# Kernel optimization log

Hardware: AMD Instinct MI355X
Metric: run time of the kernel (lower is better)

## Reference

```python
import jax, jax.numpy as jnp
import numpy as np

NSAMPLE = 32
EPS = 1e-5


def _fps(xyz, npoint):
    # xyz: [B, N, 3] -> indices [B, npoint] (farthest point sampling, start at idx 0)
    B, N, _ = xyz.shape
    def body(i, state):
        idx, dist, far = state
        idx = idx.at[:, i].set(far)
        centroid = jnp.take_along_axis(xyz, far[:, None, None], axis=1)  # [B,1,3]
        d = jnp.sum((xyz - centroid) ** 2, axis=-1)                      # [B,N]
        dist = jnp.minimum(dist, d)
        far = jnp.argmax(dist, axis=-1).astype(jnp.int32)
        return idx, dist, far
    idx0 = jnp.zeros((B, npoint), jnp.int32)
    dist0 = jnp.full((B, N), 1e10, xyz.dtype)
    far0 = jnp.zeros((B,), jnp.int32)
    idx, _, _ = jax.lax.fori_loop(0, npoint, body, (idx0, dist0, far0))
    return idx


def _knn(query, ref, k):
    # query [B,S,3], ref [B,N,3] -> neighbor idx [B,S,k]
    d = (jnp.sum(query * query, -1)[:, :, None]
         - 2.0 * jnp.einsum('bsc,bnc->bsn', query, ref)
         + jnp.sum(ref * ref, -1)[:, None, :])
    _, idx = jax.lax.top_k(-d, k)
    return idx


def _gather(x, idx):
    # x [B,N,C], idx [B,S,K] -> [B,S,K,C]
    B, S, K = idx.shape
    out = jnp.take_along_axis(x, idx.reshape(B, S * K)[..., None], axis=1)
    return out.reshape(B, S, K, x.shape[-1])


def _set_abstraction(xyz, feat, npoint, weights):
    # xyz [B,N,3], feat [B,N,C]
    fidx = _fps(xyz, npoint)
    new_xyz = jnp.take_along_axis(xyz, fidx[..., None], axis=1)        # [B,S,3]
    nidx = _knn(new_xyz, xyz, NSAMPLE)                                 # [B,S,K]
    g_xyz = _gather(xyz, nidx) - new_xyz[:, :, None, :]                # [B,S,K,3]
    g_feat = _gather(feat, nidx)                                       # [B,S,K,C]
    x = jnp.concatenate([g_xyz, g_feat], axis=-1)                      # [B,S,K,3+C]
    for W in weights:  # 1x1 conv == per-point matmul, then InstanceNorm2d (affine=False) + ReLU
        x = jnp.einsum('bskc,cd->bskd', x, W)
        mu = jnp.mean(x, axis=(1, 2), keepdims=True)
        var = jnp.var(x, axis=(1, 2), keepdims=True)
        x = jax.nn.relu((x - mu) * jax.lax.rsqrt(var + EPS))
    new_feat = jnp.max(x, axis=2)                                      # [B,S,Cout]
    return new_xyz, new_feat, fidx


def setup_inputs() -> dict:
    key = jax.random.key(0)
    ks = jax.random.split(key, 8)
    B, N = 4, 16384
    pc = jax.random.normal(ks[0], (B, 3, N), jnp.float32)
    feature = jax.random.normal(ks[1], (B, 3, N), jnp.float32)
    def w(k, cin, cout):
        return jax.random.normal(k, (cin, cout), jnp.float32) / np.sqrt(cin).astype(np.float32)
    return {
        'pc': pc, 'feature': feature,
        'sa1_w1': w(ks[2], 6, 32),  'sa1_w2': w(ks[3], 32, 32), 'sa1_w3': w(ks[4], 32, 32),
        'sa2_w1': w(ks[5], 35, 64), 'sa2_w2': w(ks[6], 64, 64), 'sa2_w3': w(ks[7], 64, 64),
    }


def reference(pc, feature, sa1_w1, sa1_w2, sa1_w3, sa2_w1, sa2_w2, sa2_w3):
    NPOINT = 4096
    xyz = jnp.transpose(pc, (0, 2, 1))       # [B,N,3]
    feat = jnp.transpose(feature, (0, 2, 1))  # [B,N,3]
    xyz1, feat1, fidx1 = _set_abstraction(xyz, feat, NPOINT // 2, [sa1_w1, sa1_w2, sa1_w3])
    xyz2, feat2, fidx2 = _set_abstraction(xyz1, feat1, NPOINT // 4, [sa2_w1, sa2_w2, sa2_w3])
    # match torch channel-first layout on outputs
    pc_l1 = jnp.transpose(xyz1, (0, 2, 1))
    pc_l2 = jnp.transpose(xyz2, (0, 2, 1))
    feat_l2 = jnp.transpose(feat2, (0, 2, 1))  # [B,64,NPOINT//4]
    return (pc, pc_l1, pc_l2, feat_l2, fidx1, fidx2)
```

## Files before the change

### kernel.cpp

```cpp
#include <hip/hip_runtime.h>
#include <math.h>

namespace {

constexpr int BB = 4;
constexpr int N0 = 16384;
constexpr int S1 = 2048;
constexpr int S2 = 1024;

__device__ __forceinline__ float sq3(float x, float y, float z){
  #pragma clang fp contract(off)
  return x*x + y*y + z*z;
}
__device__ __forceinline__ float sqdist(float ax,float ay,float az,float bx,float by,float bz){
  #pragma clang fp contract(off)
  float dx = ax-bx; float dy = ay-by; float dz = az-bz;
  return dx*dx + dy*dy + dz*dz;
}
__device__ __forceinline__ float dot3(float ax,float ay,float az,float bx,float by,float bz){
  #pragma clang fp contract(off)
  return ax*bx + ay*by + az*bz;
}
__device__ __forceinline__ float knndist(float qs, float dot, float rs){
  #pragma clang fp contract(off)
  return (qs - 2.0f*dot) + rs;
}

__global__ __launch_bounds__(256) void k_setup(const float* __restrict__ pc,
                                               const float* __restrict__ feat,
                                               float* __restrict__ out_pc,
                                               float* __restrict__ xyz,
                                               float* __restrict__ fN,
                                               float* __restrict__ rsq0)
{
  int t = blockIdx.x*256 + threadIdx.x;
  if (t < BB*3*N0) out_pc[t] = pc[t];
  if (t < BB*N0){
    int b = t >> 14, n = t & (N0-1);
    const float* p = pc + (size_t)b*3*N0;
    float x = p[n], y = p[N0+n], z = p[2*N0+n];
    float* q = xyz + (size_t)t*3;
    q[0]=x; q[1]=y; q[2]=z;
    rsq0[t] = sq3(x,y,z);
    const float* f = feat + (size_t)b*3*N0;
    float* g = fN + (size_t)t*3;
    g[0]=f[n]; g[1]=f[N0+n]; g[2]=f[2*N0+n];
  }
}

__device__ __forceinline__ void fps_writeout(int b, int i, float cx, float cy, float cz, int far,
                                             float* sxyz, float* srsq, float* pcl, float* fidxf, int NP)
{
  fidxf[(size_t)b*NP + i] = (float)far;
  float* o = sxyz + ((size_t)b*NP + i)*3;
  o[0]=cx; o[1]=cy; o[2]=cz;
  float* pb = pcl + (size_t)b*3*NP;
  pb[i] = cx; pb[NP+i] = cy; pb[2*NP+i] = cz;
  srsq[(size_t)b*NP + i] = sq3(cx,cy,cz);
}

template<int N, int NP, int BS, int PPT>
__global__ __launch_bounds__(BS) void k_fps(const float* __restrict__ pts,
                                            float* __restrict__ sxyz,
                                            float* __restrict__ srsq,
                                            float* __restrict__ pcl,
                                            float* __restrict__ fidxf)
{
  static_assert(N == BS*PPT, "bad fps shape");
  int b = blockIdx.x, t = threadIdx.x;
  const float* P = pts + (size_t)b*N*3;
  float px[PPT], py[PPT], pz[PPT], dist[PPT];
  #pragma unroll
  for (int j=0;j<PPT;j++){
    int g = t + BS*j;
    px[j]=P[g*3]; py[j]=P[g*3+1]; pz[j]=P[g*3+2];
    dist[j]=1e10f;
  }
  __shared__ unsigned s_maxbits;
  __shared__ int      s_win;
  __shared__ float    s_lo;
  float cx = P[0], cy = P[1], cz = P[2];
  if (t == 0){
    s_maxbits = 0u;
    s_win = 0x7FFFFFFF;
    fps_writeout(b, 0, cx, cy, cz, 0, sxyz, srsq, pcl, fidxf, NP);
  }
  __syncthreads();
  for (int i=1;i<NP;i++){
    float vmax = -1.0f;
    #pragma unroll
    for (int j=0;j<PPT;j++){
      float d  = sqdist(px[j],py[j],pz[j],cx,cy,cz);
      float nd = fminf(dist[j], d);
      dist[j]  = nd;
      vmax = fmaxf(vmax, nd);
    }
    #pragma unroll
    for (int off=32; off>0; off>>=1) vmax = fmaxf(vmax, __shfl_down(vmax, off));
    if ((t & 63) == 0) atomicMax(&s_maxbits, __float_as_uint(vmax));
    __syncthreads();
    if (t == 0){
      unsigned mb = s_maxbits;
      float s = sqrtf(__uint_as_float(mb));
      unsigned xb = mb;
      while (xb > 0u && sqrtf(__uint_as_float(xb - 1u)) == s) xb--;
      s_lo = __uint_as_float(xb);
      s_maxbits = 0u;
      s_win = 0x7FFFFFFF;
    }
    __syncthreads();
    float lo = s_lo;
    int li = 0x7FFFFFFF;
    #pragma unroll
    for (int j=PPT-1;j>=0;j--) if (dist[j] >= lo) li = t + BS*j;
    if (li != 0x7FFFFFFF) atomicMin(&s_win, li);
    __syncthreads();
    int far = s_win;
    cx = P[(size_t)far*3]; cy = P[(size_t)far*3+1]; cz = P[(size_t)far*3+2];
    if (t == 0) fps_writeout(b, i, cx, cy, cz, far, sxyz, srsq, pcl, fidxf, NP);
  }
}

template<int NREF, int PPT, int NQ>
__global__ __launch_bounds__(512) void k_knn(const float* __restrict__ qxyz,
                                             const float* __restrict__ qrsq,
                                             const float* __restrict__ rxyz,
                                             const float* __restrict__ rrsq,
                                             int* __restrict__ nidx)
{
  static_assert(NREF == 512*PPT, "bad knn shape");
  int q = blockIdx.x;
  int b = q / NQ;
  int t = threadIdx.x;
  const float* R  = rxyz + (size_t)b*NREF*3;
  const float* RS = rrsq + (size_t)b*NREF;
  float qx = qxyz[(size_t)q*3], qy = qxyz[(size_t)q*3+1], qz = qxyz[(size_t)q*3+2];
  float qs = qrsq[q];
  unsigned u[PPT];
  #pragma unroll
  for (int j=0;j<PPT;j++){
    int g = t + 512*j;
    float rx=R[g*3], ry=R[g*3+1], rz=R[g*3+2];
    float d = knndist(qs, dot3(qx,qy,qz,rx,ry,rz), RS[g]);
    unsigned bu = __float_as_uint(d);
    u[j] = ((int)bu < 0) ? ~bu : (bu | 0x80000000u);
  }
  __shared__ unsigned hist[256];
  __shared__ unsigned s_pref, s_pm, s_want, s_cnteq;
  __shared__ int s_n;
  __shared__ int s_eq[1024];
  __shared__ int s_ne;
  if (t == 0){ s_pref=0u; s_pm=0u; s_want=32u; s_n=0; s_ne=0; }

  for (int shift=24; shift>=0; shift-=8){
    if (t < 256) hist[t] = 0u;
    __syncthreads();
    unsigned pref = s_pref, pm = s_pm;
    #pragma unroll
    for (int j=0;j<PPT;j++){
      if ((u[j] & pm) == pref) atomicAdd(&hist[(u[j]>>shift)&255], 1u);
    }
    __syncthreads();
    if (t < 64){
      unsigned h0=hist[4*t], h1=hist[4*t+1], h2=hist[4*t+2], h3=hist[4*t+3];
      unsigned ssum = h0+h1+h2+h3;
      unsigned inc = ssum;
      #pragma unroll
      for (int off=1; off<64; off<<=1){
        unsigned o = __shfl_up(inc, off);
        if (t >= off) inc += o;
      }
      unsigned exc = inc - ssum;
      unsigned want = s_want;
      if (exc < want && want <= inc){
        unsigned rem = want - exc;
        unsigned bin, below;
        if      (rem <= h0)       { bin=4*t+0; below=exc; }
        else if (rem <= h0+h1)    { bin=4*t+1; below=exc+h0; }
        else if (rem <= h0+h1+h2) { bin=4*t+2; below=exc+h0+h1; }
        else                      { bin=4*t+3; below=exc+h0+h1+h2; }
        s_pref = pref | (bin << shift);
        s_pm   = pm   | (0xFFu << shift);
        s_want = want - below;
        if (shift == 0) s_cnteq = hist[bin];
      }
    }
    __syncthreads();
  }
  unsigned T = s_pref;
  unsigned krem = s_want;
  unsigned cnteq = s_cnteq;
  int* outq = nidx + (size_t)q*32;
  #pragma unroll
  for (int j=0;j<PPT;j++){
    if (u[j] < T){ int p = atomicAdd(&s_n, 1); outq[p] = t + 512*j; }
  }
  __syncthreads();
  if (cnteq == krem){
    #pragma unroll
    for (int j=0;j<PPT;j++){
      if (u[j] == T){ int p = atomicAdd(&s_n, 1); outq[p] = t + 512*j; }
    }
  } else {
    #pragma unroll
    for (int j=0;j<PPT;j++){
      if (u[j] == T){ int p = atomicAdd(&s_ne, 1); if (p < 1024) s_eq[p] = t + 512*j; }
    }
    __syncthreads();
    if (t == 0){
      int ne = s_ne; if (ne > 1024) ne = 1024;
      int p = s_n;
      int take = (int)krem; if (take > ne) take = ne;
      for (int r=0; r<take; r++){
        int mn = 0x7FFFFFFF, mi = -1;
        for (int e=0; e<ne; e++){ if (s_eq[e] < mn){ mn = s_eq[e]; mi = e; } }
        if (mi < 0) break;
        outq[p++] = mn;
        s_eq[mi] = 0x7FFFFFFF;
      }
    }
  }
}

template<int C>
__device__ __forceinline__ void accum_sums(const float* o, int b, float* sums){
  __shared__ float s_sum[C];
  __shared__ float s_ssq[C];
  int t = threadIdx.x;
  if (t < C){ s_sum[t]=0.f; s_ssq[t]=0.f; }
  __syncthreads();
  int lane = t & 63;
  #pragma unroll
  for (int c=0;c<C;c++){
    float v = o[c], v2 = v*v;
    #pragma unroll
    for (int off=32; off>0; off>>=1){ v += __shfl_down(v, off); v2 += __shfl_down(v2, off); }
    if (lane == 0){ atomicAdd(&s_sum[c], v); atomicAdd(&s_ssq[c], v2); }
  }
  __syncthreads();
  if (t < C){
    atomicAdd(&sums[(b*64+t)*2],   s_sum[t]);
    atomicAdd(&sums[(b*64+t)*2+1], s_ssq[t]);
  }
}

__global__ __launch_bounds__(256) void k_sa1_l1(const float* __restrict__ xyz,
                                                const float* __restrict__ fN,
                                                const float* __restrict__ sxyz,
                                                const int* __restrict__ nidx,
                                                const float* __restrict__ W,
                                                float* __restrict__ xout,
                                                float* __restrict__ sums)
{
  __shared__ float sW[192];
  int t = threadIdx.x;
  if (t < 192) sW[t] = W[t];
  int row = blockIdx.x*256 + t;
  int b = row >> 16;
  int sk = row & 65535;
  int s = sk >> 5;
  int nb = nidx[row];
  const float* pr = xyz  + ((size_t)(b*N0 + nb))*3;
  const float* pq = sxyz + ((size_t)(b*S1 + s ))*3;
  const float* pf = fN   + ((size_t)(b*N0 + nb))*3;
  float i0 = pr[0]-pq[0], i1 = pr[1]-pq[1], i2 = pr[2]-pq[2];
  float i3 = pf[0], i4 = pf[1], i5 = pf[2];
  __syncthreads();
  float o[32];
  #pragma unroll
  for (int c=0;c<32;c++){
    float a = i0*sW[c];
    a = fmaf(i1, sW[ 32+c], a);
    a = fmaf(i2, sW[ 64+c], a);
    a = fmaf(i3, sW[ 96+c], a);
    a = fmaf(i4, sW[128+c], a);
    a = fmaf(i5, sW[160+c], a);
    o[c] = a;
    xout[(size_t)c*262144 + row] = a;
  }
  accum_sums<32>(o, b, sums);
}

template<int CIN, int COUT, int LRPB>
__global__ __launch_bounds__(256) void k_sa_mid(const float* __restrict__ xin,
                                                const float* __restrict__ W,
                                                const float* __restrict__ sums_in,
                                                float* __restrict__ xout,
                                                float* __restrict__ sums_out,
                                                int rows_total, float invM)
{
  __shared__ float sW[CIN*COUT];
  __shared__ float s_mu[CIN];
  __shared__ float s_rs[CIN];
  int t = threadIdx.x;
  int row = blockIdx.x*256 + t;
  int bb = (blockIdx.x*256) >> LRPB;
  for (int i=t; i<CIN*COUT; i+=256) sW[i] = W[i];
  if (t < CIN){
    float sm = sums_in[(bb*64+t)*2], sq = sums_in[(bb*64+t)*2+1];
    float mu = sm*invM;
    float var = fmaxf(sq*invM - mu*mu, 0.f);
    s_mu[t] = mu;
    s_rs[t] = 1.0f/sqrtf(var + 1e-5f);
  }
  __syncthreads();
  float o[COUT];
  #pragma unroll
  for (int d=0;d<COUT;d++) o[d] = 0.f;
  #pragma unroll
  for (int c=0;c<CIN;c++){
    float x = xin[(size_t)c*rows_total + row];
    float v = fmaxf((x - s_mu[c])*s_rs[c], 0.f);
    #pragma unroll
    for (int d=0;d<COUT;d++) o[d] = fmaf(v, sW[c*COUT+d], o[d]);
  }
  #pragma unroll
  for (int d=0;d<COUT;d++) xout[(size_t)d*rows_total + row] = o[d];
  accum_sums<COUT>(o, bb, sums_out);
}

__global__ __launch_bounds__(256) void k_sa2_l1(const float* __restrict__ xyz1,
                                                const float* __restrict__ feat1,
                                                const float* __restrict__ xyz2,
                                                const int* __restrict__ nidx,
                                                const float* __restrict__ W,
                                                float* __restrict__ xout,
                                                float* __restrict__ sums)
{
  __shared__ float sW[35*64];
  int t = threadIdx.x;
  for (int i=t; i<35*64; i+=256) sW[i] = W[i];
  int row = blockIdx.x*256 + t;
  int b = row >> 15;
  int sk = row & 32767;
  int s = sk >> 5;
  int nb = nidx[row];
  const float* pr = xyz1 + ((size_t)(b*S1 + nb))*3;
  const float* pq = xyz2 + ((size_t)(b*S2 + s ))*3;
  const float* pf = feat1 + ((size_t)(b*S1 + nb))*32;
  float i0 = pr[0]-pq[0], i1 = pr[1]-pq[1], i2 = pr[2]-pq[2];
  float fv[32];
  #pragma unroll
  for (int c=0;c<32;c++) fv[c] = pf[c];
  __syncthreads();
  float o[64];
  #pragma unroll
  for (int d=0;d<64;d++){
    float a = i0*sW[d];
    a = fmaf(i1, sW[ 64+d], a);
    a = fmaf(i2, sW[128+d], a);
    o[d] = a;
  }
  #pragma unroll
  for (int c=0;c<32;c++){
    float v = fv[c];
    #pragma unroll
    for (int d=0;d<64;d++) o[d] = fmaf(v, sW[(3+c)*64+d], o[d]);
  }
  #pragma unroll
  for (int d=0;d<64;d++) xout[(size_t)d*131072 + row] = o[d];
  accum_sums<64>(o, b, sums);
}

template<int C, int PTSB, int CF>
__global__ __launch_bounds__(256) void k_pool(const float* __restrict__ xin,
                                              const float* __restrict__ sums_in,
                                              float* __restrict__ out,
                                              int rows_total, float invM)
{
  int t = threadIdx.x;
  int c = t & (C-1);
  int pl = t / C;
  int p = blockIdx.x*(256/C) + pl;
  int b = p / PTSB;
  float sm = sums_in[(b*64+c)*2], sq = sums_in[(b*64+c)*2+1];
  float mu = sm*invM;
  float var = fmaxf(sq*invM - mu*mu, 0.f);
  float rs = 1.0f/sqrtf(var + 1e-5f);
  const float* xp = xin + (size_t)c*rows_total + (size_t)p*32;
  float m = -1e30f;
  #pragma unroll
  for (int k=0;k<32;k++) m = fmaxf(m, xp[k]);
  m = fmaxf((m - mu)*rs, 0.0f);
  if (CF) out[((size_t)(b*C + c))*PTSB + (p - b*PTSB)] = m;
  else    out[(size_t)p*C + c] = m;
}

constexpr size_t WS_XYZ   = 0;
constexpr size_t WS_FN    = WS_XYZ   + 196608;
constexpr size_t WS_RSQ0  = WS_FN    + 196608;
constexpr size_t WS_XYZ1  = WS_RSQ0  + 65536;
constexpr size_t WS_RSQ1  = WS_XYZ1  + 24576;
constexpr size_t WS_XYZ2  = WS_RSQ1  + 8192;
constexpr size_t WS_RSQ2  = WS_XYZ2  + 12288;
constexpr size_t WS_FEAT1 = WS_RSQ2  + 4096;
constexpr size_t WS_SUMS  = WS_FEAT1 + 262144;
constexpr size_t WS_BUFA  = WS_SUMS  + 3072;
constexpr size_t WS_BUFB  = WS_BUFA  + 8388608;
constexpr size_t WS_NIDX1 = WS_BUFB  + 8388608;
constexpr size_t WS_NIDX2 = WS_NIDX1 + 262144;

constexpr size_t OUT1 = 196608;
constexpr size_t OUT2 = 221184;
constexpr size_t OUT3 = 233472;
constexpr size_t OUT4 = 495616;
constexpr size_t OUT5 = 503808;

}

extern "C" void kernel_launch(void* const* d_in, const int* in_sizes, int n_in,
                              void* d_out, int out_size, void* d_ws, size_t ws_size,
                              hipStream_t stream)
{
  (void)in_sizes; (void)n_in; (void)out_size; (void)ws_size;
  const float* pc   = (const float*)d_in[0];
  const float* feat = (const float*)d_in[1];
  const float* W1 = (const float*)d_in[2];
  const float* W2 = (const float*)d_in[3];
  const float* W3 = (const float*)d_in[4];
  const float* W4 = (const float*)d_in[5];
  const float* W5 = (const float*)d_in[6];
  const float* W6 = (const float*)d_in[7];
  float* out = (float*)d_out;
  float* ws  = (float*)d_ws;

  float* xyz   = ws + WS_XYZ;
  float* fN    = ws + WS_FN;
  float* rsq0  = ws + WS_RSQ0;
  float* xyz1  = ws + WS_XYZ1;
  float* rsq1  = ws + WS_RSQ1;
  float* xyz2  = ws + WS_XYZ2;
  float* rsq2  = ws + WS_RSQ2;
  float* feat1 = ws + WS_FEAT1;
  float* sums  = ws + WS_SUMS;
  float* bufA  = ws + WS_BUFA;
  float* bufB  = ws + WS_BUFB;
  int* nidx1   = (int*)(ws + WS_NIDX1);
  int* nidx2   = (int*)(ws + WS_NIDX2);

  (void)hipMemsetAsync(sums, 0, 3072*sizeof(float), stream);

  k_setup<<<768, 256, 0, stream>>>(pc, feat, out, xyz, fN, rsq0);

  k_fps<N0, S1, 1024, 16><<<BB, 1024, 0, stream>>>(xyz, xyz1, rsq1, out+OUT1, out+OUT4);
  k_knn<N0, 32, S1><<<BB*S1, 512, 0, stream>>>(xyz1, rsq1, xyz, rsq0, nidx1);
  k_sa1_l1<<<1024, 256, 0, stream>>>(xyz, fN, xyz1, nidx1, W1, bufA, sums);
  k_sa_mid<32,32,16><<<1024, 256, 0, stream>>>(bufA, W2, sums,       bufB, sums+512,  262144, 1.0f/65536.0f);
  k_sa_mid<32,32,16><<<1024, 256, 0, stream>>>(bufB, W3, sums+512,   bufA, sums+1024, 262144, 1.0f/65536.0f);
  k_pool<32, 2048, 0><<<1024, 256, 0, stream>>>(bufA, sums+1024, feat1, 262144, 1.0f/65536.0f);

  k_fps<S1, S2, 256, 8><<<BB, 256, 0, stream>>>(xyz1, xyz2, rsq2, out+OUT2, out+OUT5);
  k_knn<S1, 4, S2><<<BB*S2, 512, 0, stream>>>(xyz2, rsq2, xyz1, rsq1, nidx2);
  k_sa2_l1<<<512, 256, 0, stream>>>(xyz1, feat1, xyz2, nidx2, W4, bufB, sums+1536);
  k_sa_mid<64,64,15><<<512, 256, 0, stream>>>(bufB, W5, sums+1536, bufA, sums+2048, 131072, 1.0f/32768.0f);
  k_sa_mid<64,64,15><<<512, 256, 0, stream>>>(bufA, W6, sums+2048, bufB, sums+2560, 131072, 1.0f/32768.0f);
  k_pool<64, 1024, 1><<<1024, 256, 0, stream>>>(bufB, sums+2560, out+OUT3, 131072, 1.0f/32768.0f);
}
```

Measured before the change: 6.417 ms.

## Double-buffer FPS reduction state to cut a barrier and pass winner coords via LDS

Restructures the farthest-point-sampling iteration so every thread computes the sqrt-tie threshold itself instead of thread 0 doing it behind an extra barrier. Shared reduction slots are double-buffered by iteration parity, which drops one __syncthreads per iteration. Candidate winners also publish their coordinates to LDS so the next centroid is usually read from shared memory rather than from global memory. Inline asm moves are added to keep point coordinates in VGPRs. The cost is redundant per-thread tie-loop work and extra shared atomics.

```diff
diff --git a/kernel.cpp b/kernel.cpp
--- a/kernel.cpp
+++ b/kernel.cpp
@@ -73,20 +73,27 @@
   #pragma unroll
   for (int j=0;j<PPT;j++){
     int g = t + BS*j;
-    px[j]=P[g*3]; py[j]=P[g*3+1]; pz[j]=P[g*3+2];
-    dist[j]=1e10f;
-  }
-  __shared__ unsigned s_maxbits;
-  __shared__ int      s_win;
-  __shared__ float    s_lo;
+    float x = P[g*3], y = P[g*3+1], z = P[g*3+2];
+    asm volatile("v_mov_b32 %0, %1" : "=v"(px[j]) : "v"(x));
+    asm volatile("v_mov_b32 %0, %1" : "=v"(py[j]) : "v"(y));
+    asm volatile("v_mov_b32 %0, %1" : "=v"(pz[j]) : "v"(z));
+    dist[j] = 1e10f;
+  }
+  __shared__ unsigned s_maxbits[2];
+  __shared__ int s_win[2];
+  __shared__ int s_nc[2];
+  __shared__ int   s_cidx[2][16];
+  __shared__ float s_cx[2][16], s_cy[2][16], s_cz[2][16];
   float cx = P[0], cy = P[1], cz = P[2];
   if (t == 0){
-    s_maxbits = 0u;
-    s_win = 0x7FFFFFFF;
+    s_maxbits[0]=0u; s_maxbits[1]=0u;
+    s_win[0]=0x7FFFFFFF; s_win[1]=0x7FFFFFFF;
+    s_nc[0]=0; s_nc[1]=0;
     fps_writeout(b, 0, cx, cy, cz, 0, sxyz, srsq, pcl, fidxf, NP);
   }
   __syncthreads();
   for (int i=1;i<NP;i++){
+    int p = i & 1;
     float vmax = -1.0f;
     #pragma unroll
     for (int j=0;j<PPT;j++){
@@ -95,28 +102,35 @@
       dist[j]  = nd;
       vmax = fmaxf(vmax, nd);
     }
-    #pragma unroll
-    for (int off=32; off>0; off>>=1) vmax = fmaxf(vmax, __shfl_down(vmax, off));
-    if ((t & 63) == 0) atomicMax(&s_maxbits, __float_as_uint(vmax));
-    __syncthreads();
-    if (t == 0){
-      unsigned mb = s_maxbits;
-      float s = sqrtf(__uint_as_float(mb));
-      unsigned xb = mb;
-      while (xb > 0u && sqrtf(__uint_as_float(xb - 1u)) == s) xb--;
-      s_lo = __uint_as_float(xb);
-      s_maxbits = 0u;
-      s_win = 0x7FFFFFFF;
-    }
-    __syncthreads();
-    float lo = s_lo;
-    int li = 0x7FFFFFFF;
-    #pragma unroll
-    for (int j=PPT-1;j>=0;j--) if (dist[j] >= lo) li = t + BS*j;
-    if (li != 0x7FFFFFFF) atomicMin(&s_win, li);
-    __syncthreads();
-    int far = s_win;
-    cx = P[(size_t)far*3]; cy = P[(size_t)far*3+1]; cz = P[(size_t)far*3+2];
+    float wmax = vmax;
+    #pragma unroll
+    for (int off=32; off>0; off>>=1) wmax = fmaxf(wmax, __shfl_down(wmax, off));
+    if ((t & 63) == 0) atomicMax(&s_maxbits[p], __float_as_uint(wmax));
+    __syncthreads();
+    if (t == 0){ s_maxbits[1-p]=0u; s_win[1-p]=0x7FFFFFFF; s_nc[1-p]=0; }
+    unsigned mb = s_maxbits[p];
+    float s = sqrtf(__uint_as_float(mb));
+    unsigned xb = mb;
+    while (xb > 0u && sqrtf(__uint_as_float(xb-1u)) == s) xb--;
+    float lo = __uint_as_float(xb);
+    if (vmax >= lo){
+      int li = 0x7FFFFFFF; float wx=0.f, wy=0.f, wz=0.f;
+      #pragma unroll
+      for (int j=PPT-1;j>=0;j--){
+        if (dist[j] >= lo){ li = t + BS*j; wx=px[j]; wy=py[j]; wz=pz[j]; }
+      }
+      atomicMin(&s_win[p], li);
+      int sl = atomicAdd(&s_nc[p], 1);
+      if (sl < 16){ s_cidx[p][sl]=li; s_cx[p][sl]=wx; s_cy[p][sl]=wy; s_cz[p][sl]=wz; }
+    }
+    __syncthreads();
+    int far = s_win[p];
+    int nc = s_nc[p]; if (nc > 16) nc = 16;
+    bool found = false;
+    for (int k2=0;k2<nc;k2++){
+      if (s_cidx[p][k2] == far){ cx=s_cx[p][k2]; cy=s_cy[p][k2]; cz=s_cz[p][k2]; found=true; }
+    }
+    if (!found){ cx=P[(size_t)far*3]; cy=P[(size_t)far*3+1]; cz=P[(size_t)far*3+2]; }
     if (t == 0) fps_writeout(b, i, cx, cy, cz, far, sxyz, srsq, pcl, fidxf, NP);
   }
 }
```

Result: slower. 6.832 ms (+6.5%).
